# Kernel tuning notes

Measured on AMD Instinct MI355X. Metric: run time of the kernel, lower is better.

Reference implementation:

```python
import jax, jax.numpy as jnp
import numpy as np

EPS = 1e-5


def conv1x1(x, w, b=None):
    # x: [B,C,H,W], w: [O,C] (1x1 conv kernel squeezed)
    y = jnp.einsum('bchw,oc->bohw', x, w)
    if b is not None:
        y = y + b[None, :, None, None]
    return y


def bn_inf(x, g, b, m, v):
    scale = g / jnp.sqrt(v + EPS)
    return (x - m[None, :, None, None]) * scale[None, :, None, None] + b[None, :, None, None]


def setup_inputs() -> dict:
    B, C, H, W = 2, 256, 80, 80
    Ck, Cv, Co = 64, 128, 256
    key = jax.random.key(0)
    ks = jax.random.split(key, 16)
    d = {}
    d['x'] = jax.random.normal(ks[0], (B, C, H, W), dtype=jnp.float32)
    d['y'] = jax.random.normal(ks[1], (B, C, H, W), dtype=jnp.float32)
    s = 1.0 / np.sqrt(C)
    d['fk_w'] = jax.random.normal(ks[2], (Ck, C), dtype=jnp.float32) * s
    d['fk_g'] = jnp.ones((Ck,), jnp.float32)
    d['fk_b'] = jnp.zeros((Ck,), jnp.float32)
    d['fk_m'] = jax.random.normal(ks[3], (Ck,), dtype=jnp.float32) * 0.1
    d['fk_v'] = jax.random.uniform(ks[4], (Ck,), minval=0.5, maxval=1.5, dtype=jnp.float32)
    d['fq_w'] = jax.random.normal(ks[5], (Ck, C), dtype=jnp.float32) * s
    d['fq_g'] = jnp.ones((Ck,), jnp.float32)
    d['fq_b'] = jnp.zeros((Ck,), jnp.float32)
    d['fq_m'] = jax.random.normal(ks[6], (Ck,), dtype=jnp.float32) * 0.1
    d['fq_v'] = jax.random.uniform(ks[7], (Ck,), minval=0.5, maxval=1.5, dtype=jnp.float32)
    d['fv_w'] = jax.random.normal(ks[8], (Cv, C), dtype=jnp.float32) * s
    d['fv_b'] = jnp.zeros((Cv,), jnp.float32)
    d['W_w'] = jax.random.normal(ks[9], (Co, Cv), dtype=jnp.float32) * (1.0 / np.sqrt(Cv))
    d['W_b'] = jnp.zeros((Co,), jnp.float32)
    d['gamma'] = jnp.array([0.5], jnp.float32)
    return d


def reference(x, y, fk_w, fk_g, fk_b, fk_m, fk_v, fq_w, fq_g, fq_b, fq_m, fq_v, fv_w, fv_b, W_w, W_b, gamma):
    B, C, H, W = x.shape
    Ck = fk_w.shape[0]
    Cv = fv_w.shape[0]
    N = H * W
    # key from x, query/value from y (1x1 conv + BN projections)
    k = bn_inf(conv1x1(x, fk_w), fk_g, fk_b, fk_m, fk_v).reshape(B, Ck, N)          # [B,Ck,N]
    q = bn_inf(conv1x1(y, fq_w), fq_g, fq_b, fq_m, fq_v).reshape(B, Ck, N)          # [B,Ck,N]
    v = conv1x1(y, fv_w, fv_b).reshape(B, Cv, N)                                     # [B,Cv,N]
    sim = jnp.einsum('bkn,bkm->bnm', q, k) * (Ck ** -0.5)                            # [B,N,N]
    sim = jax.nn.softmax(sim, axis=-1)
    ctx = jnp.einsum('bnm,bvm->bvn', sim, v).reshape(B, Cv, H, W)                    # [B,Cv,H,W]
    ctx = conv1x1(ctx, W_w, W_b)                                                     # [B,Co,H,W]
    return gamma[0] * ctx + x
```

## Files before the change

kernel.cpp:

```cpp
#include <hip/hip_runtime.h>
#include <math.h>

#define NB   2
#define CIN  256
#define NN   6400
#define CKd  64
#define CVd  128
#define COd  256

using bf16   = __bf16;
using bf16x4 = __attribute__((ext_vector_type(4))) bf16;
using bf16x8 = __attribute__((ext_vector_type(8))) bf16;
using f32x4  = __attribute__((ext_vector_type(4))) float;

__device__ __forceinline__ void lds_cp16(const bf16* g, bf16* l) {
    __builtin_amdgcn_global_load_lds((const __attribute__((address_space(1))) void*)g,
                                     (__attribute__((address_space(3))) void*)l, 16, 0, 0);
}

__global__ void prep_kernel(const float* __restrict__ fk_w, const float* __restrict__ fk_g,
                            const float* __restrict__ fk_b, const float* __restrict__ fk_m,
                            const float* __restrict__ fk_v,
                            const float* __restrict__ fq_w, const float* __restrict__ fq_g,
                            const float* __restrict__ fq_b, const float* __restrict__ fq_m,
                            const float* __restrict__ fq_v,
                            const float* __restrict__ fv_w, const float* __restrict__ fv_b,
                            const float* __restrict__ W_w,  const float* __restrict__ W_b,
                            bf16* __restrict__ wkb, bf16* __restrict__ wqb,
                            bf16* __restrict__ wvb, bf16* __restrict__ wob,
                            float* __restrict__ bias)
{
    const int idx = blockIdx.x * 256 + threadIdx.x;
    if (idx < 16384) {
        const int co = idx >> 8;
        const float a = fk_g[co] * rsqrtf(fk_v[co] + 1e-5f);
        wkb[idx] = (bf16)(fk_w[idx] * a);
    } else if (idx < 32768) {
        const int i = idx - 16384, co = i >> 8;
        const float a = fq_g[co] * rsqrtf(fq_v[co] + 1e-5f) * 0.125f;
        wqb[i] = (bf16)(fq_w[i] * a);
    } else if (idx < 65536) {
        const int i = idx - 32768;
        wvb[i] = (bf16)fv_w[i];
    } else if (idx < 98304) {
        const int i = idx - 65536;
        wob[i] = (bf16)W_w[i];
    } else if (idx < 98816) {
        const int j = idx - 98304;
        if (j < 64)       { const float a = fk_g[j] * rsqrtf(fk_v[j] + 1e-5f); bias[j] = fk_b[j] - fk_m[j] * a; }
        else if (j < 128) { const int c = j - 64; const float a = fq_g[c] * rsqrtf(fq_v[c] + 1e-5f); bias[j] = (fq_b[c] - fq_m[c] * a) * 0.125f; }
        else if (j < 256) bias[j] = fv_b[j - 128];
        else              bias[j] = W_b[j - 256];
    }
}

__launch_bounds__(256)
__global__ void tcvt_kernel(const float* __restrict__ x, const float* __restrict__ y,
                            bf16* __restrict__ xT, bf16* __restrict__ yT)
{
    __shared__ __align__(16) bf16 t_lds[64][68];
    const int b = blockIdx.z & 1;
    const float* src = (blockIdx.z >> 1) ? y : x;
    bf16* dst = (blockIdx.z >> 1) ? yT : xT;
    const int n0 = blockIdx.x * 64, c0 = blockIdx.y * 64;
    const int tid = threadIdx.x;
    const int nl = (tid & 15) * 4;
#pragma unroll
    for (int p = 0; p < 4; ++p) {
        const int cl = (tid >> 4) + p * 16;
        const float4 v = *(const float4*)(src + (size_t)(b * CIN + c0 + cl) * NN + n0 + nl);
        t_lds[nl + 0][cl] = (bf16)v.x;
        t_lds[nl + 1][cl] = (bf16)v.y;
        t_lds[nl + 2][cl] = (bf16)v.z;
        t_lds[nl + 3][cl] = (bf16)v.w;
    }
    __syncthreads();
#pragma unroll
    for (int p = 0; p < 4; ++p) {
        const int u = tid + p * 256;
        const int n = u >> 4, c4 = (u & 15) * 4;
        const bf16x4 pk = *(const bf16x4*)&t_lds[n][c4];
        *(bf16x4*)(dst + ((size_t)b * NN + n0 + n) * CIN + c0 + c4) = pk;
    }
}

__launch_bounds__(256, 2)
__global__ void projkqv_kernel(const bf16* __restrict__ xT, const bf16* __restrict__ yT,
                               const bf16* __restrict__ wkb, const bf16* __restrict__ wqb,
                               const bf16* __restrict__ wvb, const float* __restrict__ bias,
                               bf16* __restrict__ kb, bf16* __restrict__ qb, bf16* __restrict__ vb)
{
    __shared__ __align__(16) bf16 sbuf[64 * 256];
    __shared__ __align__(16) bf16 wbuf[64 * 256];

    const int tid  = threadIdx.x;
    const int lane = tid & 63, wav = tid >> 6;
    const int l15  = lane & 15, quad = lane >> 4;
    const int b    = blockIdx.z, m = blockIdx.y;
    const int n0   = blockIdx.x * 64;

    const bf16* srcg = ((m == 0) ? xT : yT) + ((size_t)b * NN + n0) * CIN;
    const bf16* wg   = (m == 0) ? wkb : (m == 1) ? wqb : (wvb + (size_t)(m - 2) * 64 * CIN);

    const int r2  = lane >> 5;
    const int c32 = lane & 31;
#pragma unroll
    for (int i = 0; i < 8; ++i) {
        const int rg = wav * 16 + i * 2;
        const int r  = rg + r2;
        const int cs = c32 ^ (r & 7);
        lds_cp16(srcg + (size_t)r * 256 + cs * 8, &sbuf[rg * 256]);
        lds_cp16(wg   + (size_t)r * 256 + cs * 8, &wbuf[rg * 256]);
    }
    __syncthreads();

    const int key = l15 & 7;
    f32x4 acc[4];
#pragma unroll
    for (int j = 0; j < 4; ++j) acc[j] = (f32x4){0.f, 0.f, 0.f, 0.f};

    if (m < 2) {
        const int arow = wav * 16 + l15;
#pragma unroll
        for (int k4 = 0; k4 < 32; k4 += 4) {
            const bf16x8 af = *(const bf16x8*)&sbuf[arow * 256 + ((k4 + quad) ^ key) * 8];
#pragma unroll
            for (int nt = 0; nt < 4; ++nt) {
                const int brow = nt * 16 + l15;
                const bf16x8 bfw = *(const bf16x8*)&wbuf[brow * 256 + ((k4 + quad) ^ key) * 8];
                acc[nt] = __builtin_amdgcn_mfma_f32_16x16x32_bf16(af, bfw, acc[nt], 0, 0, 0);
            }
        }
        const float* bs = bias + m * 64;
        bf16* dst = (m == 0) ? kb : qb;
        const int nb = n0 + wav * 16;
#pragma unroll
        for (int nt = 0; nt < 4; ++nt) {
            const float bv = bs[nt * 16 + l15];
#pragma unroll
            for (int r = 0; r < 4; ++r) {
                const int n = nb + quad * 4 + r;
                dst[((size_t)b * NN + n) * CKd + nt * 16 + l15] = (bf16)(acc[nt][r] + bv);
            }
        }
    } else {
        const int arow = wav * 16 + l15;
#pragma unroll
        for (int k4 = 0; k4 < 32; k4 += 4) {
            const bf16x8 af = *(const bf16x8*)&wbuf[arow * 256 + ((k4 + quad) ^ key) * 8];
#pragma unroll
            for (int nt = 0; nt < 4; ++nt) {
                const int brow = nt * 16 + l15;
                const bf16x8 bfy = *(const bf16x8*)&sbuf[brow * 256 + ((k4 + quad) ^ key) * 8];
                acc[nt] = __builtin_amdgcn_mfma_f32_16x16x32_bf16(af, bfy, acc[nt], 0, 0, 0);
            }
        }
        const int cv0 = (m - 2) * 64 + wav * 16;
#pragma unroll
        for (int r = 0; r < 4; ++r) {
            const int cv = cv0 + quad * 4 + r;
            const float bv = bias[128 + cv];
#pragma unroll
            for (int nt = 0; nt < 4; ++nt)
                vb[((size_t)b * CVd + cv) * NN + n0 + nt * 16 + l15] = (bf16)(acc[nt][r] + bv);
        }
    }
}

__launch_bounds__(256, 3)
__global__ void attn_kernel(const bf16* __restrict__ qb, const bf16* __restrict__ kb,
                            const bf16* __restrict__ vb,
                            bf16* __restrict__ pO, float* __restrict__ pl,
                            int tpc, int kmask, int kbits)
{
    __shared__ __align__(16) bf16 kbuf[64 * 64];
    __shared__ __align__(16) bf16 vbuf[128 * 64];
    __shared__ __align__(16) bf16 p_lds[4][2][16][64];

    const int lane = threadIdx.x & 63;
    const int wav  = threadIdx.x >> 6;
    const int l15  = lane & 15;
    const int quad = lane >> 4;
    const int r8   = lane >> 3;
    const int c_st = lane & 7;
    const int c_src = c_st ^ r8;
    const int sw   = l15 & 7;
    const int pkey = (l15 & 7) << 1;

    const int id    = blockIdx.x;
    const int ks    = id & kmask;
    const int b     = (id >> kbits) & 1;
    const int qtile = id >> (kbits + 1);
    const int q0    = qtile * 128 + wav * 32;

    const bf16* qrow = qb + (size_t)b * NN * CKd;
    const bf16* krow = kb + (size_t)b * NN * CKd;
    const bf16* vrow = vb + (size_t)b * CVd * NN;

    bf16x8 qf[2][2];
#pragma unroll
    for (int qt = 0; qt < 2; ++qt)
#pragma unroll
        for (int s = 0; s < 2; ++s)
            qf[qt][s] = *(const bf16x8*)(qrow + (size_t)(q0 + qt * 16 + l15) * CKd + s * 32 + quad * 8);

    f32x4 acc[2][8];
#pragma unroll
    for (int qt = 0; qt < 2; ++qt)
#pragma unroll
        for (int cv = 0; cv < 8; ++cv) acc[qt][cv] = (f32x4){0.f, 0.f, 0.f, 0.f};
    float psum[2] = {0.f, 0.f};

    const int t0  = ks * tpc;
    const int rem = 100 - t0;
    const int nt  = (tpc < rem) ? tpc : rem;

    for (int t = 0; t < nt; ++t) {
        const int key0 = (t0 + t) * 64;

        __syncthreads();
        lds_cp16(krow + (size_t)(key0 + wav * 8 + r8) * CKd + c_src * 8,
                 &kbuf[(wav * 8) * 64]);
        lds_cp16(krow + (size_t)(key0 + (wav + 4) * 8 + r8) * CKd + c_src * 8,
                 &kbuf[((wav + 4) * 8) * 64]);
#pragma unroll
        for (int g4 = 0; g4 < 4; ++g4) {
            const int g = wav * 4 + g4;
            lds_cp16(vrow + (size_t)(g * 8 + r8) * NN + key0 + c_src * 8,
                     &vbuf[(g * 8) * 64]);
        }
        __syncthreads();

        f32x4 s4[2][4];
#pragma unroll
        for (int kt = 0; kt < 4; ++kt) {
            const int rr = kt * 16 + l15;
            const bf16x8 kf0 = *(const bf16x8*)&kbuf[rr * 64 + ((quad ^ sw) * 8)];
            const bf16x8 kf1 = *(const bf16x8*)&kbuf[rr * 64 + (((4 + quad) ^ sw) * 8)];
#pragma unroll
            for (int qt = 0; qt < 2; ++qt) {
                f32x4 z = (f32x4){0.f, 0.f, 0.f, 0.f};
                z = __builtin_amdgcn_mfma_f32_16x16x32_bf16(kf0, qf[qt][0], z, 0, 0, 0);
                z = __builtin_amdgcn_mfma_f32_16x16x32_bf16(kf1, qf[qt][1], z, 0, 0, 0);
                s4[qt][kt] = z;
            }
        }

#pragma unroll
        for (int qt = 0; qt < 2; ++qt) {
            float ps = 0.f;
#pragma unroll
            for (int kt = 0; kt < 4; ++kt) {
                bf16x4 pk;
#pragma unroll
                for (int r = 0; r < 4; ++r) {
                    const float p = exp2f(fmaf(s4[qt][kt][r], 1.4426950408889634f, -11.541560327111707f));
                    ps += p;
                    pk[r] = (bf16)p;
                }
                *(bf16x4*)&p_lds[wav][qt][l15][((kt * 4 + quad) ^ pkey) * 4] = pk;
            }
            psum[qt] += ps;
        }

        bf16x8 pf[2][2];
#pragma unroll
        for (int qt = 0; qt < 2; ++qt)
#pragma unroll
            for (int sp = 0; sp < 2; ++sp)
                pf[qt][sp] = *(const bf16x8*)&p_lds[wav][qt][l15][((sp * 8 + quad * 2) ^ pkey) * 4];

#pragma unroll
        for (int sp = 0; sp < 2; ++sp)
#pragma unroll
            for (int cvt = 0; cvt < 8; ++cvt) {
                const int rr = cvt * 16 + l15;
                const bf16x8 vf = *(const bf16x8*)&vbuf[rr * 64 + (((sp * 4 + quad) ^ sw) * 8)];
                acc[0][cvt] = __builtin_amdgcn_mfma_f32_16x16x32_bf16(vf, pf[0][sp], acc[0][cvt], 0, 0, 0);
                acc[1][cvt] = __builtin_amdgcn_mfma_f32_16x16x32_bf16(vf, pf[1][sp], acc[1][cvt], 0, 0, 0);
            }
    }

    __syncthreads();
    bf16* tbuf = &p_lds[wav][0][0][0];
    const size_t pb = (size_t)ks * NB + b;
#pragma unroll
    for (int qt = 0; qt < 2; ++qt) {
        psum[qt] += __shfl_xor(psum[qt], 16);
        psum[qt] += __shfl_xor(psum[qt], 32);
#pragma unroll
        for (int cvt = 0; cvt < 8; ++cvt) {
            bf16x4 pk;
#pragma unroll
            for (int r = 0; r < 4; ++r) pk[r] = (bf16)acc[qt][cvt][r];
            const int u = (cvt * 4 + quad) ^ ((l15 & 15) << 1);
            *(bf16x4*)&tbuf[l15 * 128 + u * 4] = pk;
        }
#pragma unroll
        for (int j = 0; j < 4; ++j) {
            const int row = j * 4 + (lane >> 4);
            const int g   = ((lane & 15) * 2) ^ ((row & 15) << 1);
            const bf16x8 vv = *(const bf16x8*)&tbuf[row * 128 + g * 4];
            *(bf16x8*)(pO + (pb * NN + q0 + qt * 16) * CVd + j * 512 + lane * 8) = vv;
        }
        if (quad == 0) pl[pb * NN + q0 + qt * 16 + l15] = psum[qt];
    }
}

__global__ void combine_kernel(const bf16* __restrict__ pO, const float* __restrict__ pl,
                               bf16* __restrict__ ctxT, int KS)
{
    const int idx = blockIdx.x * 256 + threadIdx.x;
    const int c4  = (idx & 31) * 4;
    const int rest = idx >> 5;
    const int n = rest % NN, b = rest / NN;

    float v0 = 0.f, v1 = 0.f, v2 = 0.f, v3 = 0.f, L = 0.f;
    for (int ks = 0; ks < KS; ++ks) {
        const size_t base = (size_t)(ks * NB + b) * NN + n;
        const bf16x4 tv = *(const bf16x4*)(pO + base * CVd + c4);
        v0 += (float)tv[0]; v1 += (float)tv[1]; v2 += (float)tv[2]; v3 += (float)tv[3];
        L += pl[base];
    }
    const float r = 1.0f / L;
    bf16x4 o;
    o[0] = (bf16)(v0 * r); o[1] = (bf16)(v1 * r); o[2] = (bf16)(v2 * r); o[3] = (bf16)(v3 * r);
    *(bf16x4*)(ctxT + ((size_t)b * NN + n) * CVd + c4) = o;
}

__launch_bounds__(256, 4)
__global__ void outproj_kernel(const bf16* __restrict__ ctxT, const bf16* __restrict__ wob,
                               const float* __restrict__ bias, const float* __restrict__ x,
                               const float* __restrict__ gam, float* __restrict__ out)
{
    const int tid  = threadIdx.x;
    const int lane = tid & 63, wav = tid >> 6;
    const int l15  = lane & 15, quad = lane >> 4;
    const int b    = blockIdx.z;
    const int co0  = blockIdx.y * 64 + wav * 16;
    const int n0   = blockIdx.x * 64;

    f32x4 acc[4];
#pragma unroll
    for (int j = 0; j < 4; ++j) acc[j] = (f32x4){0.f, 0.f, 0.f, 0.f};

    for (int kk = 0; kk < CVd; kk += 32) {
        const bf16x8 af = *(const bf16x8*)(wob + (size_t)(co0 + l15) * CVd + kk + quad * 8);
#pragma unroll
        for (int nt = 0; nt < 4; ++nt) {
            const bf16x8 bfc = *(const bf16x8*)(ctxT + ((size_t)b * NN + n0 + nt * 16 + l15) * CVd + kk + quad * 8);
            acc[nt] = __builtin_amdgcn_mfma_f32_16x16x32_bf16(af, bfc, acc[nt], 0, 0, 0);
        }
    }

    const float gm = gam[0];
#pragma unroll
    for (int r = 0; r < 4; ++r) {
        const int co = co0 + quad * 4 + r;
        const float bv = bias[256 + co];
#pragma unroll
        for (int nt = 0; nt < 4; ++nt) {
            const int n = n0 + nt * 16 + l15;
            const size_t a = ((size_t)b * COd + co) * NN + n;
            out[a] = gm * (acc[nt][r] + bv) + x[a];
        }
    }
}

extern "C" void kernel_launch(void* const* d_in, const int* in_sizes, int n_in,
                              void* d_out, int out_size, void* d_ws, size_t ws_size,
                              hipStream_t stream)
{
    const float* x     = (const float*)d_in[0];
    const float* y     = (const float*)d_in[1];
    const float* fk_w  = (const float*)d_in[2];
    const float* fk_g  = (const float*)d_in[3];
    const float* fk_b  = (const float*)d_in[4];
    const float* fk_m  = (const float*)d_in[5];
    const float* fk_v  = (const float*)d_in[6];
    const float* fq_w  = (const float*)d_in[7];
    const float* fq_g  = (const float*)d_in[8];
    const float* fq_b  = (const float*)d_in[9];
    const float* fq_m  = (const float*)d_in[10];
    const float* fq_v  = (const float*)d_in[11];
    const float* fv_w  = (const float*)d_in[12];
    const float* fv_b  = (const float*)d_in[13];
    const float* W_w   = (const float*)d_in[14];
    const float* W_b   = (const float*)d_in[15];
    const float* gamma = (const float*)d_in[16];
    float* out = (float*)d_out;

    char* ws = (char*)d_ws;
    size_t off = 0;
    auto carve = [&](size_t bytes) -> char* {
        char* p = ws + off;
        off = (off + bytes + 255) & ~(size_t)255;
        return p;
    };

    bf16*  kb   = (bf16*)carve((size_t)NB * NN * CKd * 2);
    bf16*  qbuf = (bf16*)carve((size_t)NB * NN * CKd * 2);
    bf16*  vb   = (bf16*)carve((size_t)NB * CVd * NN * 2);
    bf16*  wkb  = (bf16*)carve((size_t)CKd * CIN * 2);
    bf16*  wqb  = (bf16*)carve((size_t)CKd * CIN * 2);
    bf16*  wvb  = (bf16*)carve((size_t)CVd * CIN * 2);
    bf16*  wob  = (bf16*)carve((size_t)COd * CVd * 2);
    float* bias = (float*)carve(512 * 4);
    bf16*  ctxT = (bf16*)carve((size_t)NB * NN * CVd * 2);

    const size_t alias_start = off;
    bf16* xT = (bf16*)carve((size_t)NB * NN * CIN * 2);
    bf16* yT = (bf16*)carve((size_t)NB * NN * CIN * 2);

    const size_t region = ws_size - alias_start;
    const size_t per_ks = (size_t)NB * NN * CVd * 2 + (size_t)NB * NN * 4 + 512;
    int KS = 1, kbits = 0;
    {
        const int cand[4] = {8, 4, 2, 1};
        const int cbit[4] = {3, 2, 1, 0};
        for (int i = 0; i < 4; ++i)
            if ((size_t)cand[i] * per_ks <= region) { KS = cand[i]; kbits = cbit[i]; break; }
    }
    bf16*  pO = (bf16*)(ws + alias_start);
    float* pl = (float*)(ws + alias_start + (size_t)KS * NB * NN * CVd * 2);
    const int tpc = (100 + KS - 1) / KS;

    const dim3 blk(256);
    prep_kernel<<<386, blk, 0, stream>>>(fk_w, fk_g, fk_b, fk_m, fk_v,
                                         fq_w, fq_g, fq_b, fq_m, fq_v,
                                         fv_w, fv_b, W_w, W_b,
                                         wkb, wqb, wvb, wob, bias);
    tcvt_kernel<<<dim3(100, 4, 4), blk, 0, stream>>>(x, y, xT, yT);
    projkqv_kernel<<<dim3(100, 4, NB), blk, 0, stream>>>(xT, yT, wkb, wqb, wvb, bias, kb, qbuf, vb);
    attn_kernel<<<dim3(50 * NB * KS), blk, 0, stream>>>(qbuf, kb, vb, pO, pl, tpc, KS - 1, kbits);
    combine_kernel<<<dim3((NB * NN * CVd / 4) / 256), blk, 0, stream>>>(pO, pl, ctxT, KS);
    outproj_kernel<<<dim3(100, 4, NB), blk, 0, stream>>>(ctxT, wob, bias, x, gamma, out);
}
```

Baseline: 198.9 us.

## Double attention query tile per wave, allow non-power-of-two key splits, LDS-stage outproj

Each attention wave now processes 64 queries instead of 32, so every K/V tile loaded into LDS is reused across twice as many queries. This halves the number of query tiles and changes the key-split selection to allow 10 or 5 splits, using div/mod indexing in place of bit masks. Launch bounds drop to 2 blocks per SM because of the larger register and LDS footprint. The output projection now stages the ctx and weight tiles into swizzled LDS instead of reading them directly from global memory in the MFMA loop.

```diff
diff --git a/kernel.cpp b/kernel.cpp
--- a/kernel.cpp
+++ b/kernel.cpp
@@ -167,56 +167,54 @@
     }
 }
 
-__launch_bounds__(256, 3)
+__launch_bounds__(256, 2)
 __global__ void attn_kernel(const bf16* __restrict__ qb, const bf16* __restrict__ kb,
                             const bf16* __restrict__ vb,
-                            bf16* __restrict__ pO, float* __restrict__ pl,
-                            int tpc, int kmask, int kbits)
+                            bf16* __restrict__ pO, float* __restrict__ pl, int KS)
 {
     __shared__ __align__(16) bf16 kbuf[64 * 64];
     __shared__ __align__(16) bf16 vbuf[128 * 64];
-    __shared__ __align__(16) bf16 p_lds[4][2][16][64];
+    __shared__ __align__(16) bf16 p_lds[4][4][16][64];
 
     const int lane = threadIdx.x & 63;
     const int wav  = threadIdx.x >> 6;
     const int l15  = lane & 15;
     const int quad = lane >> 4;
     const int r8   = lane >> 3;
-    const int c_st = lane & 7;
-    const int c_src = c_st ^ r8;
+    const int c_src = (lane & 7) ^ r8;
     const int sw   = l15 & 7;
     const int pkey = (l15 & 7) << 1;
 
     const int id    = blockIdx.x;
-    const int ks    = id & kmask;
-    const int b     = (id >> kbits) & 1;
-    const int qtile = id >> (kbits + 1);
-    const int q0    = qtile * 128 + wav * 32;
+    const int ks    = id % KS;
+    const int rst   = id / KS;
+    const int b     = rst & 1;
+    const int qtile = rst >> 1;
+    const int q0    = qtile * 256 + wav * 64;
 
     const bf16* qrow = qb + (size_t)b * NN * CKd;
     const bf16* krow = kb + (size_t)b * NN * CKd;
     const bf16* vrow = vb + (size_t)b * CVd * NN;
 
-    bf16x8 qf[2][2];
-#pragma unroll
-    for (int qt = 0; qt < 2; ++qt)
+    bf16x8 qf[4][2];
+#pragma unroll
+    for (int qt = 0; qt < 4; ++qt)
 #pragma unroll
         for (int s = 0; s < 2; ++s)
             qf[qt][s] = *(const bf16x8*)(qrow + (size_t)(q0 + qt * 16 + l15) * CKd + s * 32 + quad * 8);
 
-    f32x4 acc[2][8];
-#pragma unroll
-    for (int qt = 0; qt < 2; ++qt)
+    f32x4 acc[4][8];
+#pragma unroll
+    for (int qt = 0; qt < 4; ++qt)
 #pragma unroll
         for (int cv = 0; cv < 8; ++cv) acc[qt][cv] = (f32x4){0.f, 0.f, 0.f, 0.f};
-    float psum[2] = {0.f, 0.f};
-
-    const int t0  = ks * tpc;
-    const int rem = 100 - t0;
-    const int nt  = (tpc < rem) ? tpc : rem;
-
-    for (int t = 0; t < nt; ++t) {
-        const int key0 = (t0 + t) * 64;
+    float psum[4] = {0.f, 0.f, 0.f, 0.f};
+
+    const int t0 = (100 * ks) / KS;
+    const int t1 = (100 * (ks + 1)) / KS;
+
+    for (int t = t0; t < t1; ++t) {
+        const int key0 = t * 64;
 
         __syncthreads();
         lds_cp16(krow + (size_t)(key0 + wav * 8 + r8) * CKd + c_src * 8,
@@ -231,14 +229,14 @@
         }
         __syncthreads();
 
-        f32x4 s4[2][4];
+        f32x4 s4[4][4];
 #pragma unroll
         for (int kt = 0; kt < 4; ++kt) {
             const int rr = kt * 16 + l15;
             const bf16x8 kf0 = *(const bf16x8*)&kbuf[rr * 64 + ((quad ^ sw) * 8)];
             const bf16x8 kf1 = *(const bf16x8*)&kbuf[rr * 64 + (((4 + quad) ^ sw) * 8)];
 #pragma unroll
-            for (int qt = 0; qt < 2; ++qt) {
+            for (int qt = 0; qt < 4; ++qt) {
                 f32x4 z = (f32x4){0.f, 0.f, 0.f, 0.f};
                 z = __builtin_amdgcn_mfma_f32_16x16x32_bf16(kf0, qf[qt][0], z, 0, 0, 0);
                 z = __builtin_amdgcn_mfma_f32_16x16x32_bf16(kf1, qf[qt][1], z, 0, 0, 0);
@@ -247,7 +245,7 @@
         }
 
 #pragma unroll
-        for (int qt = 0; qt < 2; ++qt) {
+        for (int qt = 0; qt < 4; ++qt) {
             float ps = 0.f;
 #pragma unroll
             for (int kt = 0; kt < 4; ++kt) {
@@ -263,9 +261,9 @@
             psum[qt] += ps;
         }
 
-        bf16x8 pf[2][2];
-#pragma unroll
-        for (int qt = 0; qt < 2; ++qt)
+        bf16x8 pf[4][2];
+#pragma unroll
+        for (int qt = 0; qt < 4; ++qt)
 #pragma unroll
             for (int sp = 0; sp < 2; ++sp)
                 pf[qt][sp] = *(const bf16x8*)&p_lds[wav][qt][l15][((sp * 8 + quad * 2) ^ pkey) * 4];
@@ -276,8 +274,9 @@
             for (int cvt = 0; cvt < 8; ++cvt) {
                 const int rr = cvt * 16 + l15;
                 const bf16x8 vf = *(const bf16x8*)&vbuf[rr * 64 + (((sp * 4 + quad) ^ sw) * 8)];
-                acc[0][cvt] = __builtin_amdgcn_mfma_f32_16x16x32_bf16(vf, pf[0][sp], acc[0][cvt], 0, 0, 0);
-                acc[1][cvt] = __builtin_amdgcn_mfma_f32_16x16x32_bf16(vf, pf[1][sp], acc[1][cvt], 0, 0, 0);
+#pragma unroll
+                for (int qt = 0; qt < 4; ++qt)
+                    acc[qt][cvt] = __builtin_amdgcn_mfma_f32_16x16x32_bf16(vf, pf[qt][sp], acc[qt][cvt], 0, 0, 0);
             }
     }
 
@@ -285,7 +284,7 @@
     bf16* tbuf = &p_lds[wav][0][0][0];
     const size_t pb = (size_t)ks * NB + b;
 #pragma unroll
-    for (int qt = 0; qt < 2; ++qt) {
+    for (int qt = 0; qt < 4; ++qt) {
         psum[qt] += __shfl_xor(psum[qt], 16);
         psum[qt] += __shfl_xor(psum[qt], 32);
 #pragma unroll
@@ -293,7 +292,7 @@
             bf16x4 pk;
 #pragma unroll
             for (int r = 0; r < 4; ++r) pk[r] = (bf16)acc[qt][cvt][r];
-            const int u = (cvt * 4 + quad) ^ ((l15 & 15) << 1);
+            const int u = (cvt * 4 + quad) ^ (l15 << 1);
             *(bf16x4*)&tbuf[l15 * 128 + u * 4] = pk;
         }
 #pragma unroll
@@ -333,30 +332,52 @@
                                const float* __restrict__ bias, const float* __restrict__ x,
                                const float* __restrict__ gam, float* __restrict__ out)
 {
+    __shared__ __align__(16) bf16 cbuf[64 * 128];
+    __shared__ __align__(16) bf16 wbuf[64 * 128];
+
     const int tid  = threadIdx.x;
     const int lane = tid & 63, wav = tid >> 6;
     const int l15  = lane & 15, quad = lane >> 4;
     const int b    = blockIdx.z;
-    const int co0  = blockIdx.y * 64 + wav * 16;
+    const int co0  = blockIdx.y * 64;
     const int n0   = blockIdx.x * 64;
 
+    const bf16* cg = ctxT + ((size_t)b * NN + n0) * CVd;
+    const bf16* wg = wob + (size_t)co0 * CVd;
+
+    const int r4  = lane >> 4;
+    const int c16 = lane & 15;
+#pragma unroll
+    for (int i = 0; i < 4; ++i) {
+        const int rg = wav * 16 + i * 4;
+        const int r  = rg + r4;
+        const int cs = c16 ^ (r & 7);
+        lds_cp16(cg + (size_t)r * 128 + cs * 8, &cbuf[rg * 128]);
+        lds_cp16(wg + (size_t)r * 128 + cs * 8, &wbuf[rg * 128]);
+    }
+    __syncthreads();
+
+    const int key = l15 & 7;
+    const int arow = wav * 16 + l15;
     f32x4 acc[4];
 #pragma unroll
     for (int j = 0; j < 4; ++j) acc[j] = (f32x4){0.f, 0.f, 0.f, 0.f};
 
-    for (int kk = 0; kk < CVd; kk += 32) {
-        const bf16x8 af = *(const bf16x8*)(wob + (size_t)(co0 + l15) * CVd + kk + quad * 8);
+#pragma unroll
+    for (int kk = 0; kk < 4; ++kk) {
+        const bf16x8 af = *(const bf16x8*)&wbuf[arow * 128 + (((kk * 4 + quad) ^ key) * 8)];
 #pragma unroll
         for (int nt = 0; nt < 4; ++nt) {
-            const bf16x8 bfc = *(const bf16x8*)(ctxT + ((size_t)b * NN + n0 + nt * 16 + l15) * CVd + kk + quad * 8);
+            const bf16x8 bfc = *(const bf16x8*)&cbuf[(nt * 16 + l15) * 128 + (((kk * 4 + quad) ^ key) * 8)];
             acc[nt] = __builtin_amdgcn_mfma_f32_16x16x32_bf16(af, bfc, acc[nt], 0, 0, 0);
         }
     }
 
     const float gm = gam[0];
+    const int cob = co0 + wav * 16;
 #pragma unroll
     for (int r = 0; r < 4; ++r) {
-        const int co = co0 + quad * 4 + r;
+        const int co = cob + quad * 4 + r;
         const float bv = bias[256 + co];
 #pragma unroll
         for (int nt = 0; nt < 4; ++nt) {
@@ -414,16 +435,14 @@
 
     const size_t region = ws_size - alias_start;
     const size_t per_ks = (size_t)NB * NN * CVd * 2 + (size_t)NB * NN * 4 + 512;
-    int KS = 1, kbits = 0;
+    int KS = 1;
     {
-        const int cand[4] = {8, 4, 2, 1};
-        const int cbit[4] = {3, 2, 1, 0};
-        for (int i = 0; i < 4; ++i)
-            if ((size_t)cand[i] * per_ks <= region) { KS = cand[i]; kbits = cbit[i]; break; }
+        const int cand[6] = {10, 8, 5, 4, 2, 1};
+        for (int i = 0; i < 6; ++i)
+            if ((size_t)cand[i] * per_ks <= region) { KS = cand[i]; break; }
     }
     bf16*  pO = (bf16*)(ws + alias_start);
     float* pl = (float*)(ws + alias_start + (size_t)KS * NB * NN * CVd * 2);
-    const int tpc = (100 + KS - 1) / KS;
 
     const dim3 blk(256);
     prep_kernel<<<386, blk, 0, stream>>>(fk_w, fk_g, fk_b, fk_m, fk_v,
@@ -432,7 +451,7 @@
                                          wkb, wqb, wvb, wob, bias);
     tcvt_kernel<<<dim3(100, 4, 4), blk, 0, stream>>>(x, y, xT, yT);
     projkqv_kernel<<<dim3(100, 4, NB), blk, 0, stream>>>(xT, yT, wkb, wqb, wvb, bias, kb, qbuf, vb);
-    attn_kernel<<<dim3(50 * NB * KS), blk, 0, stream>>>(qbuf, kb, vb, pO, pl, tpc, KS - 1, kbits);
+    attn_kernel<<<dim3(25 * NB * KS), blk, 0, stream>>>(qbuf, kb, vb, pO, pl, KS);
     combine_kernel<<<dim3((NB * NN * CVd / 4) / 256), blk, 0, stream>>>(pO, pl, ctxT, KS);
     outproj_kernel<<<dim3(100, 4, NB), blk, 0, stream>>>(ctxT, wob, bias, x, gamma, out);
 }
```

Result: faster. 193.2 us (-2.9%).

## Fuse split-K combine into output projection with LDS-staged weights

Applied to the files above, without the earlier changes.

Removes the separate combine kernel. The output projection now sums the KS partial attention outputs, normalizes them by the summed row sums, and stages the result in LDS. The full 256x128 weight matrix is also loaded into LDS through direct global-to-LDS copies with an XOR swizzle, and each block computes all 256 output channels for 32 positions. This drops one launch and the ctxT round trip to global memory, but uses about 72KB of LDS per block, which limits occupancy, and every block reloads the whole weight matrix.

```diff
diff --git a/kernel.cpp b/kernel.cpp
--- a/kernel.cpp
+++ b/kernel.cpp
@@ -13,7 +13,7 @@
 using bf16x8 = __attribute__((ext_vector_type(8))) bf16;
 using f32x4  = __attribute__((ext_vector_type(4))) float;
 
-__device__ __forceinline__ void lds_cp16(const bf16* g, bf16* l) {
+__device__ __forceinline__ void lds_cp16(const void* g, void* l) {
     __builtin_amdgcn_global_load_lds((const __attribute__((address_space(1))) void*)g,
                                      (__attribute__((address_space(3))) void*)l, 16, 0, 0);
 }
@@ -307,62 +307,102 @@
     }
 }
 
-__global__ void combine_kernel(const bf16* __restrict__ pO, const float* __restrict__ pl,
-                               bf16* __restrict__ ctxT, int KS)
-{
-    const int idx = blockIdx.x * 256 + threadIdx.x;
-    const int c4  = (idx & 31) * 4;
-    const int rest = idx >> 5;
-    const int n = rest % NN, b = rest / NN;
-
-    float v0 = 0.f, v1 = 0.f, v2 = 0.f, v3 = 0.f, L = 0.f;
-    for (int ks = 0; ks < KS; ++ks) {
-        const size_t base = (size_t)(ks * NB + b) * NN + n;
-        const bf16x4 tv = *(const bf16x4*)(pO + base * CVd + c4);
-        v0 += (float)tv[0]; v1 += (float)tv[1]; v2 += (float)tv[2]; v3 += (float)tv[3];
-        L += pl[base];
-    }
-    const float r = 1.0f / L;
-    bf16x4 o;
-    o[0] = (bf16)(v0 * r); o[1] = (bf16)(v1 * r); o[2] = (bf16)(v2 * r); o[3] = (bf16)(v3 * r);
-    *(bf16x4*)(ctxT + ((size_t)b * NN + n) * CVd + c4) = o;
-}
-
-__launch_bounds__(256, 4)
-__global__ void outproj_kernel(const bf16* __restrict__ ctxT, const bf16* __restrict__ wob,
-                               const float* __restrict__ bias, const float* __restrict__ x,
-                               const float* __restrict__ gam, float* __restrict__ out)
-{
+__launch_bounds__(256, 2)
+__global__ void outproj_kernel(const bf16* __restrict__ pO, const float* __restrict__ pl,
+                               const bf16* __restrict__ wob, const float* __restrict__ bias,
+                               const float* __restrict__ x, const float* __restrict__ gam,
+                               float* __restrict__ out, int KS)
+{
+    __shared__ __align__(16) bf16 wbuf[256 * 128];
+    __shared__ __align__(16) bf16 cbuf[32 * 128];
+    __shared__ float Lrow[32];
+
     const int tid  = threadIdx.x;
     const int lane = tid & 63, wav = tid >> 6;
     const int l15  = lane & 15, quad = lane >> 4;
-    const int b    = blockIdx.z;
-    const int co0  = blockIdx.y * 64 + wav * 16;
-    const int n0   = blockIdx.x * 64;
-
-    f32x4 acc[4];
-#pragma unroll
-    for (int j = 0; j < 4; ++j) acc[j] = (f32x4){0.f, 0.f, 0.f, 0.f};
-
-    for (int kk = 0; kk < CVd; kk += 32) {
-        const bf16x8 af = *(const bf16x8*)(wob + (size_t)(co0 + l15) * CVd + kk + quad * 8);
-#pragma unroll
-        for (int nt = 0; nt < 4; ++nt) {
-            const bf16x8 bfc = *(const bf16x8*)(ctxT + ((size_t)b * NN + n0 + nt * 16 + l15) * CVd + kk + quad * 8);
-            acc[nt] = __builtin_amdgcn_mfma_f32_16x16x32_bf16(af, bfc, acc[nt], 0, 0, 0);
+    const int b    = blockIdx.y;
+    const int n0   = blockIdx.x * 32;
+
+    {
+        const int r4 = lane >> 4;
+        const int c  = lane & 15;
+#pragma unroll
+        for (int i = 0; i < 16; ++i) {
+            const int rg = wav * 64 + i * 4;
+            const int r  = rg + r4;
+            const int cs = c ^ (r & 7);
+            lds_cp16(wob + (size_t)r * CVd + cs * 8, &wbuf[rg * 128]);
+        }
+    }
+
+    const int tn = tid >> 3;
+    const int tc = (tid & 7) * 16;
+    float vacc[16];
+#pragma unroll
+    for (int i = 0; i < 16; ++i) vacc[i] = 0.f;
+    for (int ksi = 0; ksi < KS; ++ksi) {
+        const bf16* src = pO + ((size_t)(ksi * NB + b) * NN + n0 + tn) * CVd + tc;
+#pragma unroll
+        for (int j = 0; j < 2; ++j) {
+            const bf16x8 v = *(const bf16x8*)(src + j * 8);
+#pragma unroll
+            for (int e = 0; e < 8; ++e) vacc[j * 8 + e] += (float)v[e];
+        }
+    }
+    if (tid < 32) {
+        float L = 0.f;
+        for (int ksi = 0; ksi < KS; ++ksi)
+            L += pl[(size_t)(ksi * NB + b) * NN + n0 + tid];
+        Lrow[tid] = 1.0f / L;
+    }
+    __syncthreads();
+    {
+        const float rL = Lrow[tn];
+#pragma unroll
+        for (int j = 0; j < 2; ++j) {
+            bf16x8 o;
+#pragma unroll
+            for (int e = 0; e < 8; ++e) o[e] = (bf16)(vacc[j * 8 + e] * rL);
+            const int c = (tid & 7) * 2 + j;
+            *(bf16x8*)&cbuf[tn * 128 + ((c ^ (tn & 7)) * 8)] = o;
+        }
+    }
+    __syncthreads();
+
+    f32x4 acc[4][2];
+#pragma unroll
+    for (int i = 0; i < 4; ++i)
+#pragma unroll
+        for (int j = 0; j < 2; ++j) acc[i][j] = (f32x4){0.f, 0.f, 0.f, 0.f};
+
+#pragma unroll
+    for (int kk = 0; kk < 4; ++kk) {
+#pragma unroll
+        for (int cot = 0; cot < 4; ++cot) {
+            const int arow = wav * 64 + cot * 16 + l15;
+            const bf16x8 af = *(const bf16x8*)&wbuf[arow * 128 + (((kk * 4 + quad) ^ (arow & 7)) * 8)];
+#pragma unroll
+            for (int nt = 0; nt < 2; ++nt) {
+                const int brow = nt * 16 + l15;
+                const bf16x8 bfc = *(const bf16x8*)&cbuf[brow * 128 + (((kk * 4 + quad) ^ (brow & 7)) * 8)];
+                acc[cot][nt] = __builtin_amdgcn_mfma_f32_16x16x32_bf16(af, bfc, acc[cot][nt], 0, 0, 0);
+            }
         }
     }
 
     const float gm = gam[0];
 #pragma unroll
-    for (int r = 0; r < 4; ++r) {
-        const int co = co0 + quad * 4 + r;
-        const float bv = bias[256 + co];
-#pragma unroll
-        for (int nt = 0; nt < 4; ++nt) {
-            const int n = n0 + nt * 16 + l15;
-            const size_t a = ((size_t)b * COd + co) * NN + n;
-            out[a] = gm * (acc[nt][r] + bv) + x[a];
+    for (int cot = 0; cot < 4; ++cot) {
+#pragma unroll
+        for (int r = 0; r < 4; ++r) {
+            const int co = wav * 64 + cot * 16 + quad * 4 + r;
+            const float bv = bias[256 + co];
+#pragma unroll
+            for (int nt = 0; nt < 2; ++nt) {
+                const int n = n0 + nt * 16 + l15;
+                const size_t a = ((size_t)b * COd + co) * NN + n;
+                out[a] = gm * (acc[cot][nt][r] + bv) + x[a];
+            }
         }
     }
 }
@@ -406,7 +446,6 @@
     bf16*  wvb  = (bf16*)carve((size_t)CVd * CIN * 2);
     bf16*  wob  = (bf16*)carve((size_t)COd * CVd * 2);
     float* bias = (float*)carve(512 * 4);
-    bf16*  ctxT = (bf16*)carve((size_t)NB * NN * CVd * 2);
 
     const size_t alias_start = off;
     bf16* xT = (bf16*)carve((size_t)NB * NN * CIN * 2);
@@ -433,6 +472,5 @@
     tcvt_kernel<<<dim3(100, 4, 4), blk, 0, stream>>>(x, y, xT, yT);
     projkqv_kernel<<<dim3(100, 4, NB), blk, 0, stream>>>(xT, yT, wkb, wqb, wvb, bias, kb, qbuf, vb);
     attn_kernel<<<dim3(50 * NB * KS), blk, 0, stream>>>(qbuf, kb, vb, pO, pl, tpc, KS - 1, kbits);
-    combine_kernel<<<dim3((NB * NN * CVd / 4) / 256), blk, 0, stream>>>(pO, pl, ctxT, KS);
-    outproj_kernel<<<dim3(100, 4, NB), blk, 0, stream>>>(ctxT, wob, bias, x, gamma, out);
-}
+    outproj_kernel<<<dim3(200, NB), blk, 0, stream>>>(pO, pl, wob, bias, x, gamma, out, KS);
+}
```

New measurement: 192.4 us. -3.3%, faster.
